# Optimization experiments

Measured on AMD Instinct MI355X. Metric: run time of the kernel, lower is better.

## Reference

```python
import jax, jax.numpy as jnp
import numpy as np

B, H, W, DIM = 2, 256, 256, 256
PDIM, HEADS = 128, 8
CH = PDIM // HEADS  # per-head channel dim (16)


def _dwconv3x3(x, w):
    # x: [b, c, h, w], w: [c, 1, 3, 3], depthwise (groups=c)
    return jax.lax.conv_general_dilated(
        x, w, window_strides=(1, 1), padding=((1, 1), (1, 1)),
        dimension_numbers=("NCHW", "OIHW", "NCHW"),
        feature_group_count=w.shape[0])


def setup_inputs() -> dict:
    key = jax.random.key(0)
    ks = jax.random.split(key, 8)

    def nrm(k, shape, fan):
        return jax.random.normal(k, shape, jnp.float32) / np.float32(np.sqrt(fan))

    x = jax.random.normal(ks[0], (B, H, W, DIM), jnp.float32)
    qkv_w = nrm(ks[1], (3 * PDIM, PDIM), PDIM)            # 1x1 conv, no bias
    dw_w = nrm(ks[2], (3 * PDIM, 1, 3, 3), 9)             # depthwise 3x3, no bias
    proj_w = nrm(ks[3], (DIM, DIM), DIM)                  # 1x1 conv, no bias
    g1_w = nrm(ks[4], (DIM // 2, DIM), DIM)               # gate conv1 (bias=True default)
    g1_b = jnp.zeros((DIM // 2,), jnp.float32)
    g2_w = nrm(ks[5], (1, DIM // 2), DIM // 2)            # gate conv2
    g2_b = jnp.zeros((1,), jnp.float32)
    temperature = jnp.ones((HEADS, 1, 1), jnp.float32)
    attn1 = jnp.array([0.2], jnp.float32)
    attn2 = jnp.array([0.2], jnp.float32)
    attn3 = jnp.array([0.2], jnp.float32)
    attn4 = jnp.array([0.2], jnp.float32)
    return dict(x=x, qkv_w=qkv_w, dw_w=dw_w, proj_w=proj_w, g1_w=g1_w,
                g1_b=g1_b, g2_w=g2_w, g2_b=g2_b, temperature=temperature,
                attn1=attn1, attn2=attn2, attn3=attn3, attn4=attn4)


def reference(x, qkv_w, dw_w, proj_w, g1_w, g1_b, g2_w, g2_b,
              temperature, attn1, attn2, attn3, attn4):
    xc = jnp.transpose(x, (0, 3, 1, 2))  # [b, dim, h, w]
    b, c, h, w = xc.shape
    x1, x2 = xc[:, :PDIM], xc[:, PDIM:]

    qkv = jnp.einsum('oc,bchw->bohw', qkv_w, x1)
    qkv = _dwconv3x3(qkv, dw_w)
    q, k, v = jnp.split(qkv, 3, axis=1)

    def to_heads(t):
        return t.reshape(b, HEADS, CH, h * w)  # [b, head, C, hw]

    q, k, v = to_heads(q), to_heads(k), to_heads(v)
    q = q / jnp.maximum(jnp.linalg.norm(q, axis=-1, keepdims=True), 1e-12)
    k = k / jnp.maximum(jnp.linalg.norm(k, axis=-1, keepdims=True), 1e-12)

    # gate -> scalar dynamic_k = int(C * mean(sigmoid(...)))
    g = jax.nn.relu(jnp.einsum('oc,bchw->bohw', g1_w, xc) + g1_b[None, :, None, None])
    g = jax.nn.sigmoid(jnp.einsum('oc,bchw->bohw', g2_w, g) + g2_b[None, :, None, None])
    dyn_k = jax.lax.stop_gradient(jnp.floor(CH * jnp.mean(g)))  # scalar float, grad-stopped like int()

    attn = jnp.einsum('bhcn,bhdn->bhcd', q, k) * temperature  # [b, head, C, C]
    # top-k mask via rank: rank[i,j] = position of attn[i,j] in descending sort of row i
    ranks = jnp.argsort(jnp.argsort(-attn, axis=-1), axis=-1)
    attn = jnp.where(ranks < dyn_k, attn, -jnp.inf)
    attn = jax.nn.softmax(attn, axis=-1)

    out_av = jnp.einsum('bhcd,bhdn->bhcn', attn, v)
    # out1..out4 are identical in the original; weighted sum collapses
    out = out_av * attn1 + out_av * attn2 + out_av * attn3 + out_av * attn4
    out = out.reshape(b, PDIM, h, w)
    out = jnp.einsum('oc,bchw->bohw', proj_w, jnp.concatenate([out, x2], axis=1))
    return jnp.transpose(out, (0, 2, 3, 1))  # [b, h, w, dim]
```

## Files before the change

### kernel.cpp

```cpp
#include <hip/hip_runtime.h>
#include <hip/hip_bf16.h>
#include <cstdint>
#include <cstddef>

typedef __attribute__((ext_vector_type(4))) float v4f;
typedef __attribute__((ext_vector_type(8))) short v8s;
typedef __attribute__((ext_vector_type(4))) short v4s;
typedef __attribute__((ext_vector_type(4))) unsigned v4u;

__device__ __forceinline__ short f2bf(float f) {
  unsigned u = __float_as_uint(f);
  u += 0x7FFFu + ((u >> 16) & 1u);
  return (short)(u >> 16);
}
__device__ __forceinline__ float bf2f(short h) {
  return __uint_as_float(((unsigned)(unsigned short)h) << 16);
}
__device__ __forceinline__ v4f mfma16(v8s a, v8s b, v4f c) {
  return __builtin_amdgcn_mfma_f32_16x16x32_bf16(a, b, c, 0, 0, 0);
}
__device__ __forceinline__ unsigned pack_rn(float a, float b) {
  __hip_bfloat162 p = __float22bfloat162_rn(make_float2(a, b));
  union { __hip_bfloat162 v; unsigned u; } c; c.v = p; return c.u;
}
struct u2 { unsigned h, l; };
__device__ __forceinline__ u2 split2pk(float a, float b) {
  const unsigned ua = __float_as_uint(a) & 0xffff0000u;
  const unsigned ub = __float_as_uint(b) & 0xffff0000u;
  const float la = a - __uint_as_float(ua);
  const float lb = b - __uint_as_float(ub);
  u2 r;
  r.h = (ua >> 16) | ub;
  r.l = pack_rn(la, lb);
  return r;
}

#define OFF_GRAM   0u
#define OFF_QN     32768u
#define OFF_KN     34816u
#define OFF_GSUM   36864u
#define OFF_ATTN   40960u
#define OFF_WQH    65536u
#define OFF_WQL    163840u
#define OFF_G1H    262144u
#define OFF_G1L    327680u
#define OFF_W2     393216u
#define OFF_QK     1048576u
#define OFF_V      135266304u
#define OFF_VOUT   168820736u

__global__ void k0_split(const float* __restrict__ qkv_w, const float* __restrict__ g1_w,
                         short* __restrict__ wqh, short* __restrict__ wql,
                         short* __restrict__ g1h, short* __restrict__ g1l) {
  const int t = blockIdx.x * 256 + threadIdx.x;
  if (t < 6144) {
    const int l = t & 63, ks = (t >> 6) & 3, g = t >> 8;
    const int n = g * 16 + (l & 15), k = ks * 32 + (l >> 4) * 8;
    v8s hi, lo;
#pragma unroll
    for (int j = 0; j < 8; ++j) {
      const float f = qkv_w[n * 128 + k + j];
      const short h = f2bf(f);
      hi[j] = h; lo[j] = f2bf(f - bf2f(h));
    }
    *(v8s*)(wqh + (size_t)t * 8) = hi;
    *(v8s*)(wql + (size_t)t * 8) = lo;
  } else if (t < 10240) {
    const int t2 = t - 6144;
    const int l = t2 & 63, ks2 = (t2 >> 6) & 7, g2 = t2 >> 9;
    const int n = g2 * 16 + (l & 15), k = ks2 * 32 + (l >> 4) * 8;
    v8s hi, lo;
#pragma unroll
    for (int j = 0; j < 8; ++j) {
      const float f = g1_w[n * 256 + k + j];
      const short h = f2bf(f);
      hi[j] = h; lo[j] = f2bf(f - bf2f(h));
    }
    *(v8s*)(g1h + (size_t)t2 * 8) = hi;
    *(v8s*)(g1l + (size_t)t2 * 8) = lo;
  }
}

__global__ __launch_bounds__(512, 4) void k1_qkv(const float* __restrict__ x,
                                                 const short* __restrict__ wqh,
                                                 const short* __restrict__ wql,
                                                 float* __restrict__ qkf,
                                                 short* __restrict__ vb) {
  __shared__ __align__(16) unsigned char sm[49152];
  const int tid = threadIdx.x;
  const size_t m0 = (size_t)blockIdx.x * 64;
  const int lane = tid & 63, wid = tid >> 6;
  const int wm = wid >> 2, wn = wid & 3;

  v8s pbh[3], pbl[3];
#pragma unroll
  for (int s = 0; s < 3; ++s) {
    const size_t off = ((size_t)((0 * 4 + wn) * 4 + s) * 64 + lane) * 8;
    pbh[s] = *(const v8s*)(wqh + off);
    pbl[s] = *(const v8s*)(wql + off);
  }

  {
    const int row = tid >> 3, c0 = (tid & 7) * 16;
    const float* src = x + (m0 + (size_t)row) * 256 + c0;
#pragma unroll
    for (int half = 0; half < 2; ++half) {
      v4f f0 = *(const v4f*)(src + half * 8);
      v4f f1 = *(const v4f*)(src + half * 8 + 4);
      v4u hi, lo;
      u2 t0 = split2pk(f0[0], f0[1]); hi[0] = t0.h; lo[0] = t0.l;
      u2 t1 = split2pk(f0[2], f0[3]); hi[1] = t1.h; lo[1] = t1.l;
      u2 t2 = split2pk(f1[0], f1[1]); hi[2] = t2.h; lo[2] = t2.l;
      u2 t3 = split2pk(f1[2], f1[3]); hi[3] = t3.h; lo[3] = t3.l;
      const int col = c0 + half * 8;
      const int byo = (row * 256 + col * 2) ^ ((row & 7) << 4);
      *(v4u*)(sm + byo) = hi;
      *(v4u*)(sm + 16384 + byo) = lo;
    }
  }
  __syncthreads();
  v8s ah[4][2];
#pragma unroll
  for (int ks = 0; ks < 4; ++ks)
#pragma unroll
    for (int mi = 0; mi < 2; ++mi) {
      const int kb2 = (ks * 32 + ((lane >> 4) * 8)) * 2;
      const int m = wm * 32 + mi * 16 + (lane & 15);
      const int byoA = (m * 256 + kb2) ^ ((m & 7) << 4);
      ah[ks][mi] = *(const v8s*)(sm + byoA);
    }
  const v4f vz = {0.f, 0.f, 0.f, 0.f};
  v4f acc[6][2];
#pragma unroll
  for (int i = 0; i < 6; ++i) { acc[i][0] = vz; acc[i][1] = vz; }

#pragma unroll
  for (int s = 0; s < 24; ++s) {
    const int nc = s >> 2, ks = s & 3, slot = s % 3;
    const v8s bh = pbh[slot];
    const v8s bl = pbl[slot];
    if (s + 3 < 24) {
      const int s3 = s + 3, nc3 = s3 >> 2, ks3 = s3 & 3;
      const size_t off = ((size_t)((nc3 * 4 + wn) * 4 + ks3) * 64 + lane) * 8;
      pbh[slot] = *(const v8s*)(wqh + off);
      if (nc3 < 4) pbl[slot] = *(const v8s*)(wql + off);
    }
#pragma unroll
    for (int mi = 0; mi < 2; ++mi) {
      const int kb2 = (ks * 32 + ((lane >> 4) * 8)) * 2;
      const int m = wm * 32 + mi * 16 + (lane & 15);
      const int byoA = (m * 256 + kb2) ^ ((m & 7) << 4);
      acc[nc][mi] = mfma16(ah[ks][mi], bh, acc[nc][mi]);
      if (nc < 4) {
        const v8s alv = *(const v8s*)(sm + 16384 + byoA);
        acc[nc][mi] = mfma16(alv, bh, acc[nc][mi]);
        acc[nc][mi] = mfma16(ah[ks][mi], bl, acc[nc][mi]);
      }
    }
  }
#pragma unroll
  for (int nc = 0; nc < 4; ++nc)
#pragma unroll
    for (int mi = 0; mi < 2; ++mi)
#pragma unroll
      for (int r = 0; r < 4; ++r) {
        const int m = wm * 32 + mi * 16 + ((lane >> 4) * 4) + r;
        const int n = nc * 64 + wn * 16 + (lane & 15);
        qkf[(m0 + m) * 256 + n] = acc[nc][mi][r];
      }
  short* vtr = (short*)(sm + 32768);
#pragma unroll
  for (int nc = 4; nc < 6; ++nc)
#pragma unroll
    for (int mi = 0; mi < 2; ++mi)
#pragma unroll
      for (int r = 0; r < 4; ++r) {
        const int m = wm * 32 + mi * 16 + ((lane >> 4) * 4) + r;
        const int n = (nc - 4) * 64 + wn * 16 + (lane & 15);
        vtr[m * 128 + n] = f2bf(acc[nc][mi][r]);
      }
  __syncthreads();
  {
    const int base = tid * 8;
#pragma unroll
    for (int p = 0; p < 2; ++p) {
      const int flat = p * 4096 + base;
      const int row = flat >> 7, col = flat & 127;
      const v8s t = *(const v8s*)(vtr + row * 128 + col);
      *(v8s*)(vb + (m0 + row) * 128 + col) = t;
    }
  }
}

__global__ __launch_bounds__(512, 4) void k1_g(const float* __restrict__ x,
                                               const short* __restrict__ g1h,
                                               const short* __restrict__ g1l,
                                               const float* __restrict__ g1_b,
                                               const float* __restrict__ g2_w,
                                               const float* __restrict__ g2_b,
                                               double* __restrict__ gsum) {
  __shared__ __align__(16) unsigned char sm[32768];
  const int tid = threadIdx.x;
  const size_t m0 = (size_t)blockIdx.x * 64;
  const int lane = tid & 63, wid = tid >> 6;
  const int wm = wid >> 2, wn = wid & 3;
  const v4f vz = {0.f, 0.f, 0.f, 0.f};
  v4f acc[2][2];
  acc[0][0] = vz; acc[0][1] = vz; acc[1][0] = vz; acc[1][1] = vz;
  v8s pbh[3], pbl[3];
#pragma unroll
  for (int kc = 0; kc < 2; ++kc) {
#pragma unroll
    for (int s = 0; s < 3; ++s) {
      const int nc = s >> 2, ks = s & 3;
      const size_t off = ((size_t)((nc * 4 + wn) * 8 + kc * 4 + ks) * 64 + lane) * 8;
      pbh[s] = *(const v8s*)(g1h + off);
      pbl[s] = *(const v8s*)(g1l + off);
    }
    __syncthreads();
    {
      const int row = tid >> 3, c0 = (tid & 7) * 16;
      const float* src = x + (m0 + (size_t)row) * 256 + kc * 128 + c0;
#pragma unroll
      for (int half = 0; half < 2; ++half) {
        v4f f0 = *(const v4f*)(src + half * 8);
        v4f f1 = *(const v4f*)(src + half * 8 + 4);
        v4u hi, lo;
        u2 t0 = split2pk(f0[0], f0[1]); hi[0] = t0.h; lo[0] = t0.l;
        u2 t1 = split2pk(f0[2], f0[3]); hi[1] = t1.h; lo[1] = t1.l;
        u2 t2 = split2pk(f1[0], f1[1]); hi[2] = t2.h; lo[2] = t2.l;
        u2 t3 = split2pk(f1[2], f1[3]); hi[3] = t3.h; lo[3] = t3.l;
        const int col = c0 + half * 8;
        const int byo = (row * 256 + col * 2) ^ ((row & 7) << 4);
        *(v4u*)(sm + byo) = hi;
        *(v4u*)(sm + 16384 + byo) = lo;
      }
    }
    __syncthreads();
    v8s ah[4][2];
#pragma unroll
    for (int ks = 0; ks < 4; ++ks)
#pragma unroll
      for (int mi = 0; mi < 2; ++mi) {
        const int kb2 = (ks * 32 + ((lane >> 4) * 8)) * 2;
        const int m = wm * 32 + mi * 16 + (lane & 15);
        const int byoA = (m * 256 + kb2) ^ ((m & 7) << 4);
        ah[ks][mi] = *(const v8s*)(sm + byoA);
      }
#pragma unroll
    for (int s = 0; s < 8; ++s) {
      const int nc = s >> 2, ks = s & 3, slot = s % 3;
      const v8s bh = pbh[slot];
      const v8s bl = pbl[slot];
      if (s + 3 < 8) {
        const int s3 = s + 3, nc3 = s3 >> 2, ks3 = s3 & 3;
        const size_t off = ((size_t)((nc3 * 4 + wn) * 8 + kc * 4 + ks3) * 64 + lane) * 8;
        pbh[slot] = *(const v8s*)(g1h + off);
        pbl[slot] = *(const v8s*)(g1l + off);
      }
#pragma unroll
      for (int mi = 0; mi < 2; ++mi) {
        const int kb2 = (ks * 32 + ((lane >> 4) * 8)) * 2;
        const int m = wm * 32 + mi * 16 + (lane & 15);
        const int byoA = (m * 256 + kb2) ^ ((m & 7) << 4);
        const v8s alv = *(const v8s*)(sm + 16384 + byoA);
        acc[nc][mi] = mfma16(ah[ks][mi], bh, acc[nc][mi]);
        acc[nc][mi] = mfma16(alv, bh, acc[nc][mi]);
        acc[nc][mi] = mfma16(ah[ks][mi], bl, acc[nc][mi]);
        acc[nc][mi] = mfma16(alv, bl, acc[nc][mi]);
      }
    }
  }
  __syncthreads();
  float* g2ws = (float*)sm;
  float* ldsg = (float*)(sm + 512);
  if (tid < 128) g2ws[tid] = g2_w[tid];
  if (tid < 64) ldsg[tid] = 0.f;
  __syncthreads();
  float bias[2], g2v[2];
#pragma unroll
  for (int nc = 0; nc < 2; ++nc) {
    const int n = nc * 64 + wn * 16 + (lane & 15);
    bias[nc] = g1_b[n];
    g2v[nc] = g2ws[n];
  }
#pragma unroll
  for (int mi = 0; mi < 2; ++mi)
#pragma unroll
    for (int r = 0; r < 4; ++r) {
      float part = 0.f;
#pragma unroll
      for (int nc = 0; nc < 2; ++nc) {
        float val = acc[nc][mi][r] + bias[nc];
        val = fmaxf(val, 0.f);
        part += val * g2v[nc];
      }
      part += __shfl_xor(part, 1, 16);
      part += __shfl_xor(part, 2, 16);
      part += __shfl_xor(part, 4, 16);
      part += __shfl_xor(part, 8, 16);
      if ((lane & 15) == 0)
        atomicAdd(&ldsg[wm * 32 + mi * 16 + ((lane >> 4) * 4) + r], part);
    }
  __syncthreads();
  if (tid < 64) {
    float pre = ldsg[tid] + g2_b[0];
    float g = 1.f / (1.f + expf(-pre));
#pragma unroll
    for (int mk = 1; mk < 64; mk <<= 1) g += __shfl_xor(g, mk, 64);
    if (tid == 0) atomicAdd(gsum, (double)g);
  }
}

__global__ __launch_bounds__(256, 4) void k2_conv(const float* __restrict__ qkf,
                                                  const short* __restrict__ vb,
                                                  const float* __restrict__ dw_w,
                                                  double* __restrict__ gram,
                                                  double* __restrict__ qn,
                                                  double* __restrict__ kn,
                                                  short* __restrict__ vbuf) {
  __shared__ __align__(16) unsigned char SM[28480];
  float* haloT = (float*)SM;
  short* vtr   = (short*)SM;
  float* wsm   = (float*)(SM + 23296);
  float* redQ  = (float*)(SM + 23872);
  float* redK  = (float*)(SM + 24128);
  float* gramW = (float*)(SM + 24384);

  const int tid = threadIdx.x;
  const int tile = blockIdx.x, h = blockIdx.y, b = blockIdx.z;
  const int px0 = (tile & 15) * 16, py0 = (tile >> 4) * 16;
  const int c = tid & 15, r = tid >> 4;
  const int lane = tid & 63, w4 = tid >> 6;

  auto stage_load = [&](int sec, v4f* vals) {
    const int chbase = sec * 128 + h * 16;
#pragma unroll
    for (int i = 0; i < 6; ++i) {
      const int idx = tid + i * 256;
      v4f val = {0.f, 0.f, 0.f, 0.f};
      if (idx < 1296) {
        const int p = idx >> 2, e4 = (idx & 3) * 4;
        const int row = p / 18, col = p - row * 18;
        const int gy = py0 - 1 + row, gx = px0 - 1 + col;
        if (gy >= 0 && gy < 256 && gx >= 0 && gx < 256) {
          const size_t pix = (size_t)(b * 65536 + gy * 256 + gx);
          if (sec < 2) {
            val = *(const v4f*)(qkf + pix * 256 + sec * 128 + h * 16 + e4);
          } else {
            const v4s sv = *(const v4s*)(vb + pix * 128 + h * 16 + e4);
            val[0] = bf2f(sv[0]); val[1] = bf2f(sv[1]);
            val[2] = bf2f(sv[2]); val[3] = bf2f(sv[3]);
          }
        }
      }
      vals[i] = val;
    }
  };
  auto stage_write = [&](int sec, const v4f* vals) {
#pragma unroll
    for (int i = 0; i < 6; ++i) {
      const int idx = tid + i * 256;
      if (idx < 1296) {
        const int p = idx >> 2, e4 = (idx & 3) * 4;
        const int row = p / 18, col = p - row * 18;
        haloT[(e4 + 0) * 364 + row * 20 + col] = vals[i][0];
        haloT[(e4 + 1) * 364 + row * 20 + col] = vals[i][1];
        haloT[(e4 + 2) * 364 + row * 20 + col] = vals[i][2];
        haloT[(e4 + 3) * 364 + row * 20 + col] = vals[i][3];
      }
    }
    if (tid < 144) wsm[tid] = dw_w[(sec * 128 + h * 16) * 9 + tid];
  };

  auto conv16 = [&](float* o) {
#pragma unroll
    for (int j = 0; j < 16; ++j) o[j] = 0.f;
#pragma unroll
    for (int dy = 0; dy < 3; ++dy) {
      const float* rp = haloT + c * 364 + (r + dy) * 20;
      const v4f t0 = *(const v4f*)(rp);
      const v4f t1 = *(const v4f*)(rp + 4);
      const v4f t2 = *(const v4f*)(rp + 8);
      const v4f t3 = *(const v4f*)(rp + 12);
      float rb[18];
#pragma unroll
      for (int q = 0; q < 4; ++q) { rb[q] = t0[q]; rb[4+q] = t1[q]; rb[8+q] = t2[q]; rb[12+q] = t3[q]; }
      rb[16] = rp[16]; rb[17] = rp[17];
      const float w0 = wsm[c * 9 + dy * 3 + 0];
      const float w1 = wsm[c * 9 + dy * 3 + 1];
      const float w2 = wsm[c * 9 + dy * 3 + 2];
#pragma unroll
      for (int j = 0; j < 16; ++j)
        o[j] += w0 * rb[j] + w1 * rb[j + 1] + w2 * rb[j + 2];
    }
  };

  float qreg[16], kreg[16];
  v4f sbuf[6];

  stage_load(0, sbuf);
  stage_write(0, sbuf);
  __syncthreads();
  v4f sk[6];
  stage_load(1, sk);
  conv16(qreg);
  {
    float s = 0.f;
#pragma unroll
    for (int j = 0; j < 16; ++j) s += qreg[j] * qreg[j];
    s += __shfl_xor(s, 16, 64);
    s += __shfl_xor(s, 32, 64);
    if (lane < 16) redQ[w4 * 16 + lane] = s;
  }
  __syncthreads();
  stage_write(1, sk);
  __syncthreads();
  v4f sv[6];
  stage_load(2, sv);
  conv16(kreg);
  {
    float s = 0.f;
#pragma unroll
    for (int j = 0; j < 16; ++j) s += kreg[j] * kreg[j];
    s += __shfl_xor(s, 16, 64);
    s += __shfl_xor(s, 32, 64);
    if (lane < 16) redK[w4 * 16 + lane] = s;
  }
  {
    v4f acc = {0.f, 0.f, 0.f, 0.f};
    const int qt = lane >> 4;
    const bool hiHalf = (qt & 1);
#pragma unroll
    for (int f = 0; f < 2; ++f) {
      const int src = ((f * 2 + (qt >> 1)) << 4) | (lane & 15);
      v4u qh4, ql4, kh4, kl4;
#pragma unroll
      for (int jj = 0; jj < 4; ++jj) {
        const float q0a = __shfl(qreg[2 * jj], src, 64);
        const float q0b = __shfl(qreg[2 * jj + 8], src, 64);
        const float q1a = __shfl(qreg[2 * jj + 1], src, 64);
        const float q1b = __shfl(qreg[2 * jj + 9], src, 64);
        const float k0a = __shfl(kreg[2 * jj], src, 64);
        const float k0b = __shfl(kreg[2 * jj + 8], src, 64);
        const float k1a = __shfl(kreg[2 * jj + 1], src, 64);
        const float k1b = __shfl(kreg[2 * jj + 9], src, 64);
        const float q0 = hiHalf ? q0b : q0a, q1 = hiHalf ? q1b : q1a;
        const float k0 = hiHalf ? k0b : k0a, k1 = hiHalf ? k1b : k1a;
        const u2 tq = split2pk(q0, q1); qh4[jj] = tq.h; ql4[jj] = tq.l;
        const u2 tk = split2pk(k0, k1); kh4[jj] = tk.h; kl4[jj] = tk.l;
      }
      const v8s qh = __builtin_bit_cast(v8s, qh4);
      const v8s ql = __builtin_bit_cast(v8s, ql4);
      const v8s kh = __builtin_bit_cast(v8s, kh4);
      const v8s kl = __builtin_bit_cast(v8s, kl4);
      acc = mfma16(qh, kh, acc);
      acc = mfma16(ql, kh, acc);
      acc = mfma16(qh, kl, acc);
      acc = mfma16(ql, kl, acc);
    }
#pragma unroll
    for (int rr = 0; rr < 4; ++rr)
      gramW[w4 * 256 + (qt * 4 + rr) * 16 + (lane & 15)] = acc[rr];
  }
  __syncthreads();
  stage_write(2, sv);
  __syncthreads();
  float vv[16];
  conv16(vv);
  if (tid < 16) {
    const float t = redQ[tid] + redQ[16 + tid] + redQ[32 + tid] + redQ[48 + tid];
    atomicAdd(&qn[b * 128 + h * 16 + tid], (double)t);
  } else if (tid < 32) {
    const int cc = tid - 16;
    const float t = redK[cc] + redK[16 + cc] + redK[32 + cc] + redK[48 + cc];
    atomicAdd(&kn[b * 128 + h * 16 + cc], (double)t);
  }
  {
    const float g = gramW[tid] + gramW[256 + tid] + gramW[512 + tid] + gramW[768 + tid];
    atomicAdd(&gram[(size_t)(b * 8 + h) * 256 + tid], (double)g);
  }
  __syncthreads();
  {
#pragma unroll
    for (int j = 0; j < 16; ++j) vtr[(r * 16 + j) * 24 + c] = f2bf(vv[j]);
  }
  __syncthreads();
  {
    const v8s o0 = *(const v8s*)(vtr + tid * 24);
    const v8s o1 = *(const v8s*)(vtr + tid * 24 + 8);
    short* dst = vbuf + ((size_t)b * 65536 + (size_t)(py0 + (tid >> 4)) * 256 + (px0 + (tid & 15))) * 128 + h * 16;
    *(v8s*)dst = o0;
    *(v8s*)(dst + 8) = o1;
  }
}

__global__ void k3a_attn(const double* __restrict__ gram, const double* __restrict__ qn,
                         const double* __restrict__ kn, const double* __restrict__ gsum,
                         const float* __restrict__ temp,
                         const float* __restrict__ a1p, const float* __restrict__ a2p,
                         const float* __restrict__ a3p, const float* __restrict__ a4p,
                         float* __restrict__ attnw) {
  const int t = threadIdx.x;
  const int b = t >> 7, rem = t & 127, h = rem >> 4, c = rem & 15;
  const float qnv = fmaxf(sqrtf((float)qn[b * 128 + h * 16 + c]), 1e-12f);
  const float tv = temp[h];
  float a[16];
#pragma unroll
  for (int d = 0; d < 16; ++d) {
    const float knv = fmaxf(sqrtf((float)kn[b * 128 + h * 16 + d]), 1e-12f);
    a[d] = (float)gram[(size_t)(b * 8 + h) * 256 + c * 16 + d] / (qnv * knv) * tv;
  }
  const float dynk = floorf(16.f * (float)(gsum[0] / 131072.0));
  float mx = -INFINITY;
  bool keep[16];
#pragma unroll
  for (int d = 0; d < 16; ++d) {
    int rank = 0;
#pragma unroll
    for (int e = 0; e < 16; ++e)
      rank += ((a[e] > a[d]) || ((a[e] == a[d]) && (e < d))) ? 1 : 0;
    keep[d] = ((float)rank < dynk);
    if (keep[d]) mx = fmaxf(mx, a[d]);
  }
  float ssum = 0.f, wvv[16];
#pragma unroll
  for (int d = 0; d < 16; ++d) {
    wvv[d] = keep[d] ? expf(a[d] - mx) : 0.f;
    ssum += wvv[d];
  }
  const float satt = a1p[0] + a2p[0] + a3p[0] + a4p[0];
  const float sc = satt / ssum;
#pragma unroll
  for (int d = 0; d < 16; ++d) attnw[t * 16 + d] = wvv[d] * sc;
}

__global__ void k3b_fold(const float* __restrict__ proj_w, const float* __restrict__ attnw,
                         short* __restrict__ W2f) {
  const int g = blockIdx.x, b = blockIdx.y;
  const int ks = threadIdx.x >> 6, lane = threadIdx.x & 63;
  const int o = g * 16 + (lane & 15);
  const int k0 = ks * 32 + (lane >> 4) * 8;
  v8s outv;
  if (k0 < 128) {
    const int h = k0 >> 4, d0 = k0 & 15;
    float s[8];
#pragma unroll
    for (int j = 0; j < 8; ++j) s[j] = 0.f;
#pragma unroll
    for (int i = 0; i < 16; ++i) {
      const float pw = proj_w[o * 256 + h * 16 + i];
#pragma unroll
      for (int j = 0; j < 8; ++j)
        s[j] += pw * attnw[((b * 8 + h) * 16 + i) * 16 + d0 + j];
    }
#pragma unroll
    for (int j = 0; j < 8; ++j) outv[j] = f2bf(s[j]);
  } else {
#pragma unroll
    for (int j = 0; j < 8; ++j) outv[j] = f2bf(proj_w[o * 256 + k0 + j]);
  }
  *(v8s*)(W2f + ((size_t)(b * 128 + g * 8 + ks) * 64 + lane) * 8) = outv;
}

__global__ __launch_bounds__(512, 4) void k4_out(const short* __restrict__ vbuf,
                                                 const float* __restrict__ x,
                                                 const short* __restrict__ W2f,
                                                 float* __restrict__ out) {
  __shared__ __align__(16) unsigned char sm[32768];
  const int tid = threadIdx.x;
  const size_t m0 = (size_t)blockIdx.x * 64;
  const int b = (int)(m0 >> 16);
  const int lane = tid & 63, wid = tid >> 6;
  const int wm = wid >> 2, wn = wid & 3;

  v8s pbB[3];
#pragma unroll
  for (int s = 0; s < 3; ++s) {
    const size_t off = ((size_t)(b * 128 + (0 * 4 + wn) * 8 + s) * 64 + lane) * 8;
    pbB[s] = *(const v8s*)(W2f + off);
  }
  {
    const int row = tid >> 3, c0 = (tid & 7) * 16;
    {
      const short* src = vbuf + (m0 + (size_t)row) * 128 + c0;
#pragma unroll
      for (int half = 0; half < 2; ++half) {
        const int col = c0 + half * 8;
        const int byo = (row * 512 + col * 2) ^ ((row & 7) << 4);
        *(v8s*)(sm + byo) = *(const v8s*)(src + half * 8);
      }
    }
    {
      const float* src = x + (m0 + (size_t)row) * 256 + 128 + c0;
#pragma unroll
      for (int half = 0; half < 2; ++half) {
        v4f f0 = *(const v4f*)(src + half * 8);
        v4f f1 = *(const v4f*)(src + half * 8 + 4);
        v4u hv;
        hv[0] = pack_rn(f0[0], f0[1]); hv[1] = pack_rn(f0[2], f0[3]);
        hv[2] = pack_rn(f1[0], f1[1]); hv[3] = pack_rn(f1[2], f1[3]);
        const int col = 128 + c0 + half * 8;
        const int byo = (row * 512 + col * 2) ^ ((row & 7) << 4);
        *(v4u*)(sm + byo) = hv;
      }
    }
  }
  __syncthreads();
  v8s af[8][2];
#pragma unroll
  for (int ks = 0; ks < 8; ++ks)
#pragma unroll
    for (int mi = 0; mi < 2; ++mi) {
      const int kb2 = (ks * 32 + ((lane >> 4) * 8)) * 2;
      const int m = wm * 32 + mi * 16 + (lane & 15);
      const int byoA = (m * 512 + kb2) ^ ((m & 7) << 4);
      af[ks][mi] = *(const v8s*)(sm + byoA);
    }
  const v4f vz = {0.f, 0.f, 0.f, 0.f};
  v4f acc[4][2];
#pragma unroll
  for (int i = 0; i < 4; ++i) { acc[i][0] = vz; acc[i][1] = vz; }
#pragma unroll
  for (int s = 0; s < 32; ++s) {
    const int nc = s >> 3, ks = s & 7, slot = s % 3;
    const v8s bf = pbB[slot];
    if (s + 3 < 32) {
      const int s3 = s + 3, nc3 = s3 >> 3, ks3 = s3 & 7;
      const size_t off = ((size_t)(b * 128 + (nc3 * 4 + wn) * 8 + ks3) * 64 + lane) * 8;
      pbB[slot] = *(const v8s*)(W2f + off);
    }
#pragma unroll
    for (int mi = 0; mi < 2; ++mi)
      acc[nc][mi] = mfma16(af[ks][mi], bf, acc[nc][mi]);
  }
#pragma unroll
  for (int nc = 0; nc < 4; ++nc)
#pragma unroll
    for (int mi = 0; mi < 2; ++mi)
#pragma unroll
      for (int r = 0; r < 4; ++r) {
        const int m = wm * 32 + mi * 16 + ((lane >> 4) * 4) + r;
        const int o = nc * 64 + wn * 16 + (lane & 15);
        out[(m0 + m) * 256 + o] = acc[nc][mi][r];
      }
}

extern "C" void kernel_launch(void* const* d_in, const int* in_sizes, int n_in,
                              void* d_out, int out_size, void* d_ws, size_t ws_size,
                              hipStream_t stream) {
  const float* x      = (const float*)d_in[0];
  const float* qkv_w  = (const float*)d_in[1];
  const float* dw_w   = (const float*)d_in[2];
  const float* proj_w = (const float*)d_in[3];
  const float* g1_w   = (const float*)d_in[4];
  const float* g1_b   = (const float*)d_in[5];
  const float* g2_w   = (const float*)d_in[6];
  const float* g2_b   = (const float*)d_in[7];
  const float* temp   = (const float*)d_in[8];
  const float* a1     = (const float*)d_in[9];
  const float* a2     = (const float*)d_in[10];
  const float* a3     = (const float*)d_in[11];
  const float* a4     = (const float*)d_in[12];
  float* out = (float*)d_out;
  char* ws = (char*)d_ws;

  double* gram  = (double*)(ws + OFF_GRAM);
  double* qn    = (double*)(ws + OFF_QN);
  double* kn    = (double*)(ws + OFF_KN);
  double* gsum  = (double*)(ws + OFF_GSUM);
  float*  attnw = (float*)(ws + OFF_ATTN);
  short*  wqh   = (short*)(ws + OFF_WQH);
  short*  wql   = (short*)(ws + OFF_WQL);
  short*  g1h   = (short*)(ws + OFF_G1H);
  short*  g1l   = (short*)(ws + OFF_G1L);
  short*  W2f   = (short*)(ws + OFF_W2);
  float*  qkf   = (float*)(ws + OFF_QK);
  short*  vb    = (short*)(ws + OFF_V);
  short*  vbuf  = (short*)(ws + OFF_VOUT);

  hipMemsetAsync(ws, 0, 40960, stream);
  k0_split<<<40, 256, 0, stream>>>(qkv_w, g1_w, wqh, wql, g1h, g1l);
  k1_qkv<<<2048, 512, 0, stream>>>(x, wqh, wql, qkf, vb);
  k1_g<<<2048, 512, 0, stream>>>(x, g1h, g1l, g1_b, g2_w, g2_b, gsum);
  k2_conv<<<dim3(256, 8, 2), 256, 0, stream>>>(qkf, vb, dw_w, gram, qn, kn, vbuf);
  k3a_attn<<<1, 256, 0, stream>>>(gram, qn, kn, gsum, temp, a1, a2, a3, a4, attnw);
  k3b_fold<<<dim3(16, 2), 512, 0, stream>>>(proj_w, attnw, W2f);
  k4_out<<<2048, 512, 0, stream>>>(vbuf, x, W2f, out);
  (void)in_sizes; (void)n_in; (void)out_size; (void)ws_size;
}
```

Before: 280.1 us.

## Fuse qkv projection and gate GEMM kernels into one pass over x

Merges the separate qkv 1x1-conv kernel and the gate-conv kernel into a single kernel. The first half of each x tile is split into hi/lo bf16 parts once and shared by both GEMMs, and qkv results are written per column chunk instead of being held in six accumulators. The aim is to remove a second read of x and one kernel launch. In exchange, a single block does more serialized work and register and LDS pressure may change.

```diff
diff --git a/kernel.cpp b/kernel.cpp
--- a/kernel.cpp
+++ b/kernel.cpp
@@ -81,23 +81,42 @@
   }
 }
 
-__global__ __launch_bounds__(512, 4) void k1_qkv(const float* __restrict__ x,
-                                                 const short* __restrict__ wqh,
-                                                 const short* __restrict__ wql,
-                                                 float* __restrict__ qkf,
-                                                 short* __restrict__ vb) {
+__global__ __launch_bounds__(512, 4) void k1f(const float* __restrict__ x,
+                                              const short* __restrict__ wqh,
+                                              const short* __restrict__ wql,
+                                              const short* __restrict__ g1h,
+                                              const short* __restrict__ g1l,
+                                              const float* __restrict__ g1_b,
+                                              const float* __restrict__ g2_w,
+                                              const float* __restrict__ g2_b,
+                                              float* __restrict__ qkf,
+                                              short* __restrict__ vb,
+                                              double* __restrict__ gsum) {
   __shared__ __align__(16) unsigned char sm[49152];
   const int tid = threadIdx.x;
   const size_t m0 = (size_t)blockIdx.x * 64;
   const int lane = tid & 63, wid = tid >> 6;
   const int wm = wid >> 2, wn = wid & 3;
+  short* vtr = (short*)(sm + 32768);
+
+  auto bh_ptr = [&](int s) -> const short* {
+    if (s < 8) { const int nc = s >> 2, ks = s & 3;
+      return g1h + ((size_t)((nc * 4 + wn) * 8 + ks) * 64 + lane) * 8; }
+    const int t = s - 8, nc = t >> 2, ks = t & 3;
+    return wqh + ((size_t)((nc * 4 + wn) * 4 + ks) * 64 + lane) * 8;
+  };
+  auto bl_ptr = [&](int s) -> const short* {
+    if (s < 8) { const int nc = s >> 2, ks = s & 3;
+      return g1l + ((size_t)((nc * 4 + wn) * 8 + ks) * 64 + lane) * 8; }
+    const int t = s - 8, nc = t >> 2, ks = t & 3;
+    return wql + ((size_t)((nc * 4 + wn) * 4 + ks) * 64 + lane) * 8;
+  };
 
   v8s pbh[3], pbl[3];
 #pragma unroll
   for (int s = 0; s < 3; ++s) {
-    const size_t off = ((size_t)((0 * 4 + wn) * 4 + s) * 64 + lane) * 8;
-    pbh[s] = *(const v8s*)(wqh + off);
-    pbl[s] = *(const v8s*)(wql + off);
+    pbh[s] = *(const v8s*)bh_ptr(s);
+    pbl[s] = *(const v8s*)bl_ptr(s);
   }
 
   {
@@ -130,145 +149,121 @@
       ah[ks][mi] = *(const v8s*)(sm + byoA);
     }
   const v4f vz = {0.f, 0.f, 0.f, 0.f};
-  v4f acc[6][2];
-#pragma unroll
-  for (int i = 0; i < 6; ++i) { acc[i][0] = vz; acc[i][1] = vz; }
-
-#pragma unroll
-  for (int s = 0; s < 24; ++s) {
-    const int nc = s >> 2, ks = s & 3, slot = s % 3;
+  v4f accg[2][2];
+  accg[0][0] = vz; accg[0][1] = vz; accg[1][0] = vz; accg[1][1] = vz;
+  v4f accq[2];
+
+#pragma unroll
+  for (int s = 0; s < 32; ++s) {
+    const int slot = s % 3;
     const v8s bh = pbh[slot];
     const v8s bl = pbl[slot];
-    if (s + 3 < 24) {
-      const int s3 = s + 3, nc3 = s3 >> 2, ks3 = s3 & 3;
-      const size_t off = ((size_t)((nc3 * 4 + wn) * 4 + ks3) * 64 + lane) * 8;
-      pbh[slot] = *(const v8s*)(wqh + off);
-      if (nc3 < 4) pbl[slot] = *(const v8s*)(wql + off);
-    }
-#pragma unroll
-    for (int mi = 0; mi < 2; ++mi) {
-      const int kb2 = (ks * 32 + ((lane >> 4) * 8)) * 2;
-      const int m = wm * 32 + mi * 16 + (lane & 15);
-      const int byoA = (m * 256 + kb2) ^ ((m & 7) << 4);
-      acc[nc][mi] = mfma16(ah[ks][mi], bh, acc[nc][mi]);
-      if (nc < 4) {
-        const v8s alv = *(const v8s*)(sm + 16384 + byoA);
-        acc[nc][mi] = mfma16(alv, bh, acc[nc][mi]);
-        acc[nc][mi] = mfma16(ah[ks][mi], bl, acc[nc][mi]);
-      }
-    }
-  }
-#pragma unroll
-  for (int nc = 0; nc < 4; ++nc)
-#pragma unroll
-    for (int mi = 0; mi < 2; ++mi)
-#pragma unroll
-      for (int r = 0; r < 4; ++r) {
-        const int m = wm * 32 + mi * 16 + ((lane >> 4) * 4) + r;
-        const int n = nc * 64 + wn * 16 + (lane & 15);
-        qkf[(m0 + m) * 256 + n] = acc[nc][mi][r];
-      }
-  short* vtr = (short*)(sm + 32768);
-#pragma unroll
-  for (int nc = 4; nc < 6; ++nc)
-#pragma unroll
-    for (int mi = 0; mi < 2; ++mi)
-#pragma unroll
-      for (int r = 0; r < 4; ++r) {
-        const int m = wm * 32 + mi * 16 + ((lane >> 4) * 4) + r;
-        const int n = (nc - 4) * 64 + wn * 16 + (lane & 15);
-        vtr[m * 128 + n] = f2bf(acc[nc][mi][r]);
-      }
-  __syncthreads();
-  {
-    const int base = tid * 8;
-#pragma unroll
-    for (int p = 0; p < 2; ++p) {
-      const int flat = p * 4096 + base;
-      const int row = flat >> 7, col = flat & 127;
-      const v8s t = *(const v8s*)(vtr + row * 128 + col);
-      *(v8s*)(vb + (m0 + row) * 128 + col) = t;
-    }
-  }
-}
-
-__global__ __launch_bounds__(512, 4) void k1_g(const float* __restrict__ x,
-                                               const short* __restrict__ g1h,
-                                               const short* __restrict__ g1l,
-                                               const float* __restrict__ g1_b,
-                                               const float* __restrict__ g2_w,
-                                               const float* __restrict__ g2_b,
-                                               double* __restrict__ gsum) {
-  __shared__ __align__(16) unsigned char sm[32768];
-  const int tid = threadIdx.x;
-  const size_t m0 = (size_t)blockIdx.x * 64;
-  const int lane = tid & 63, wid = tid >> 6;
-  const int wm = wid >> 2, wn = wid & 3;
-  const v4f vz = {0.f, 0.f, 0.f, 0.f};
-  v4f acc[2][2];
-  acc[0][0] = vz; acc[0][1] = vz; acc[1][0] = vz; acc[1][1] = vz;
-  v8s pbh[3], pbl[3];
-#pragma unroll
-  for (int kc = 0; kc < 2; ++kc) {
-#pragma unroll
-    for (int s = 0; s < 3; ++s) {
+    if (s + 3 < 32) {
+      const int s3 = s + 3;
+      pbh[slot] = *(const v8s*)bh_ptr(s3);
+      const bool needl = (s3 < 8) || (s3 - 8 < 16);
+      if (needl) pbl[slot] = *(const v8s*)bl_ptr(s3);
+    }
+    if (s < 8) {
       const int nc = s >> 2, ks = s & 3;
-      const size_t off = ((size_t)((nc * 4 + wn) * 8 + kc * 4 + ks) * 64 + lane) * 8;
-      pbh[s] = *(const v8s*)(g1h + off);
-      pbl[s] = *(const v8s*)(g1l + off);
-    }
-    __syncthreads();
-    {
-      const int row = tid >> 3, c0 = (tid & 7) * 16;
-      const float* src = x + (m0 + (size_t)row) * 256 + kc * 128 + c0;
-#pragma unroll
-      for (int half = 0; half < 2; ++half) {
-        v4f f0 = *(const v4f*)(src + half * 8);
-        v4f f1 = *(const v4f*)(src + half * 8 + 4);
-        v4u hi, lo;
-        u2 t0 = split2pk(f0[0], f0[1]); hi[0] = t0.h; lo[0] = t0.l;
-        u2 t1 = split2pk(f0[2], f0[3]); hi[1] = t1.h; lo[1] = t1.l;
-        u2 t2 = split2pk(f1[0], f1[1]); hi[2] = t2.h; lo[2] = t2.l;
-        u2 t3 = split2pk(f1[2], f1[3]); hi[3] = t3.h; lo[3] = t3.l;
-        const int col = c0 + half * 8;
-        const int byo = (row * 256 + col * 2) ^ ((row & 7) << 4);
-        *(v4u*)(sm + byo) = hi;
-        *(v4u*)(sm + 16384 + byo) = lo;
-      }
-    }
-    __syncthreads();
-    v8s ah[4][2];
-#pragma unroll
-    for (int ks = 0; ks < 4; ++ks)
-#pragma unroll
-      for (int mi = 0; mi < 2; ++mi) {
-        const int kb2 = (ks * 32 + ((lane >> 4) * 8)) * 2;
-        const int m = wm * 32 + mi * 16 + (lane & 15);
-        const int byoA = (m * 256 + kb2) ^ ((m & 7) << 4);
-        ah[ks][mi] = *(const v8s*)(sm + byoA);
-      }
-#pragma unroll
-    for (int s = 0; s < 8; ++s) {
-      const int nc = s >> 2, ks = s & 3, slot = s % 3;
-      const v8s bh = pbh[slot];
-      const v8s bl = pbl[slot];
-      if (s + 3 < 8) {
-        const int s3 = s + 3, nc3 = s3 >> 2, ks3 = s3 & 3;
-        const size_t off = ((size_t)((nc3 * 4 + wn) * 8 + kc * 4 + ks3) * 64 + lane) * 8;
-        pbh[slot] = *(const v8s*)(g1h + off);
-        pbl[slot] = *(const v8s*)(g1l + off);
-      }
 #pragma unroll
       for (int mi = 0; mi < 2; ++mi) {
         const int kb2 = (ks * 32 + ((lane >> 4) * 8)) * 2;
         const int m = wm * 32 + mi * 16 + (lane & 15);
         const int byoA = (m * 256 + kb2) ^ ((m & 7) << 4);
         const v8s alv = *(const v8s*)(sm + 16384 + byoA);
-        acc[nc][mi] = mfma16(ah[ks][mi], bh, acc[nc][mi]);
-        acc[nc][mi] = mfma16(alv, bh, acc[nc][mi]);
-        acc[nc][mi] = mfma16(ah[ks][mi], bl, acc[nc][mi]);
-        acc[nc][mi] = mfma16(alv, bl, acc[nc][mi]);
-      }
+        accg[nc][mi] = mfma16(ah[ks][mi], bh, accg[nc][mi]);
+        accg[nc][mi] = mfma16(alv, bh, accg[nc][mi]);
+        accg[nc][mi] = mfma16(ah[ks][mi], bl, accg[nc][mi]);
+        accg[nc][mi] = mfma16(alv, bl, accg[nc][mi]);
+      }
+    } else {
+      const int t = s - 8, nc = t >> 2, ks = t & 3;
+#pragma unroll
+      for (int mi = 0; mi < 2; ++mi) {
+        if (ks == 0) accq[mi] = vz;
+        const int kb2 = (ks * 32 + ((lane >> 4) * 8)) * 2;
+        const int m = wm * 32 + mi * 16 + (lane & 15);
+        const int byoA = (m * 256 + kb2) ^ ((m & 7) << 4);
+        accq[mi] = mfma16(ah[ks][mi], bh, accq[mi]);
+        if (nc < 4) {
+          const v8s alv = *(const v8s*)(sm + 16384 + byoA);
+          accq[mi] = mfma16(alv, bh, accq[mi]);
+          accq[mi] = mfma16(ah[ks][mi], bl, accq[mi]);
+        }
+      }
+      if (ks == 3) {
+        if (nc < 4) {
+#pragma unroll
+          for (int mi = 0; mi < 2; ++mi)
+#pragma unroll
+            for (int r = 0; r < 4; ++r) {
+              const int m = wm * 32 + mi * 16 + ((lane >> 4) * 4) + r;
+              const int n = nc * 64 + wn * 16 + (lane & 15);
+              qkf[(m0 + m) * 256 + n] = accq[mi][r];
+            }
+        } else {
+#pragma unroll
+          for (int mi = 0; mi < 2; ++mi)
+#pragma unroll
+            for (int r = 0; r < 4; ++r) {
+              const int m = wm * 32 + mi * 16 + ((lane >> 4) * 4) + r;
+              const int n = (nc - 4) * 64 + wn * 16 + (lane & 15);
+              vtr[m * 128 + n] = f2bf(accq[mi][r]);
+            }
+        }
+      }
+    }
+  }
+
+  v8s pb2h[3], pb2l[3];
+#pragma unroll
+  for (int s = 0; s < 3; ++s) {
+    const size_t off = ((size_t)((0 * 4 + wn) * 8 + 4 + s) * 64 + lane) * 8;
+    pb2h[s] = *(const v8s*)(g1h + off);
+    pb2l[s] = *(const v8s*)(g1l + off);
+  }
+  __syncthreads();
+  {
+    const int row = tid >> 3, c0 = (tid & 7) * 16;
+    const float* src = x + (m0 + (size_t)row) * 256 + 128 + c0;
+#pragma unroll
+    for (int half = 0; half < 2; ++half) {
+      v4f f0 = *(const v4f*)(src + half * 8);
+      v4f f1 = *(const v4f*)(src + half * 8 + 4);
+      v4u hi, lo;
+      u2 t0 = split2pk(f0[0], f0[1]); hi[0] = t0.h; lo[0] = t0.l;
+      u2 t1 = split2pk(f0[2], f0[3]); hi[1] = t1.h; lo[1] = t1.l;
+      u2 t2 = split2pk(f1[0], f1[1]); hi[2] = t2.h; lo[2] = t2.l;
+      u2 t3 = split2pk(f1[2], f1[3]); hi[3] = t3.h; lo[3] = t3.l;
+      const int col = c0 + half * 8;
+      const int byo = (row * 256 + col * 2) ^ ((row & 7) << 4);
+      *(v4u*)(sm + byo) = hi;
+      *(v4u*)(sm + 16384 + byo) = lo;
+    }
+  }
+  __syncthreads();
+#pragma unroll
+  for (int s = 0; s < 8; ++s) {
+    const int nc = s >> 2, ks = s & 3, slot = s % 3;
+    const v8s bh = pb2h[slot];
+    const v8s bl = pb2l[slot];
+    if (s + 3 < 8) {
+      const int s3 = s + 3, nc3 = s3 >> 2, ks3 = s3 & 3;
+      const size_t off = ((size_t)((nc3 * 4 + wn) * 8 + 4 + ks3) * 64 + lane) * 8;
+      pb2h[slot] = *(const v8s*)(g1h + off);
+      pb2l[slot] = *(const v8s*)(g1l + off);
+    }
+#pragma unroll
+    for (int mi = 0; mi < 2; ++mi) {
+      const int kb2 = (ks * 32 + ((lane >> 4) * 8)) * 2;
+      const int m = wm * 32 + mi * 16 + (lane & 15);
+      const int byoA = (m * 256 + kb2) ^ ((m & 7) << 4);
+      const v8s alv = *(const v8s*)(sm + 16384 + byoA);
+      accg[nc][mi] = mfma16(ah[ks][mi], bh, accg[nc][mi]);
+      accg[nc][mi] = mfma16(alv, bh, accg[nc][mi]);
+      accg[nc][mi] = mfma16(ah[ks][mi], bl, accg[nc][mi]);
+      accg[nc][mi] = mfma16(alv, bl, accg[nc][mi]);
     }
   }
   __syncthreads();
@@ -291,7 +286,7 @@
       float part = 0.f;
 #pragma unroll
       for (int nc = 0; nc < 2; ++nc) {
-        float val = acc[nc][mi][r] + bias[nc];
+        float val = accg[nc][mi][r] + bias[nc];
         val = fmaxf(val, 0.f);
         part += val * g2v[nc];
       }
@@ -309,6 +304,16 @@
 #pragma unroll
     for (int mk = 1; mk < 64; mk <<= 1) g += __shfl_xor(g, mk, 64);
     if (tid == 0) atomicAdd(gsum, (double)g);
+  }
+  {
+    const int base = tid * 8;
+#pragma unroll
+    for (int p = 0; p < 2; ++p) {
+      const int flat = p * 4096 + base;
+      const int row = flat >> 7, col = flat & 127;
+      const v8s t = *(const v8s*)(vtr + row * 128 + col);
+      *(v8s*)(vb + (m0 + row) * 128 + col) = t;
+    }
   }
 }
 
@@ -681,8 +686,7 @@
 
   hipMemsetAsync(ws, 0, 40960, stream);
   k0_split<<<40, 256, 0, stream>>>(qkv_w, g1_w, wqh, wql, g1h, g1l);
-  k1_qkv<<<2048, 512, 0, stream>>>(x, wqh, wql, qkf, vb);
-  k1_g<<<2048, 512, 0, stream>>>(x, g1h, g1l, g1_b, g2_w, g2_b, gsum);
+  k1f<<<2048, 512, 0, stream>>>(x, wqh, wql, g1h, g1l, g1_b, g2_w, g2_b, qkf, vb, gsum);
   k2_conv<<<dim3(256, 8, 2), 256, 0, stream>>>(qkf, vb, dw_w, gram, qn, kn, vbuf);
   k3a_attn<<<1, 256, 0, stream>>>(gram, qn, kn, gsum, temp, a1, a2, a3, a4, attnw);
   k3b_fold<<<dim3(16, 2), 512, 0, stream>>>(proj_w, attnw, W2f);
```

New measurement: 257.8 us. 8.0% less time.
